# Kernel tuning notes

Hardware: AMD Instinct MI355X
Metric: run time of the kernel (lower is better)

The kernel has to match this reference:

```python
import jax, jax.numpy as jnp
import numpy as np

B, S, D, H = 8, 512, 1024, 8
DPH = D // H            # 128, dim per head
MAX_REL = 32
NGRAM = 2               # 2-gram RNN on heads 4..7
NG_START, NG_COUNT = 4, 4
SCALE = float(DPH) ** 0.5


def setup_inputs() -> dict:
    key = jax.random.key(0)
    ks = jax.random.split(key, 12)
    w = lambda k, shp: jax.random.normal(k, shp, jnp.float32) * 0.02
    return {
        "x": jax.random.normal(ks[0], (B, S, D), jnp.float32),
        "mask": jax.random.randint(ks[1], (B, 1, S), 0, 2).astype(bool),
        "Wq": w(ks[2], (D, D)), "bq": jnp.zeros((D,), jnp.float32),
        "Wk": w(ks[3], (D, D)), "bk": jnp.zeros((D,), jnp.float32),
        "Wv": w(ks[4], (D, D)), "bv": jnp.zeros((D,), jnp.float32),
        "Wo": w(ks[5], (D, D)), "bo": jnp.zeros((D,), jnp.float32),
        "rel_emb": w(ks[6], (2 * MAX_REL + 1, DPH)),
        "Wih_f": w(ks[7], (DPH, DPH)), "Whh_f": w(ks[8], (DPH, DPH)),
        "bih_f": jnp.zeros((DPH,), jnp.float32), "bhh_f": jnp.zeros((DPH,), jnp.float32),
        "Wih_b": w(ks[9], (DPH, DPH)), "Whh_b": w(ks[10], (DPH, DPH)),
        "bih_b": jnp.zeros((DPH,), jnp.float32), "bhh_b": jnp.zeros((DPH,), jnp.float32),
    }


def reference(x, mask, Wq, bq, Wk, bk, Wv, bv, Wo, bo, rel_emb,
              Wih_f, Whh_f, bih_f, bhh_f, Wih_b, Whh_b, bih_b, bhh_b):
    shape_h = lambda t: t.reshape(B, S, H, DPH).transpose(0, 2, 1, 3)  # [B,H,S,d]
    q = shape_h(x @ Wq.T + bq)
    k = shape_h(x @ Wk.T + bk)
    v = shape_h(x @ Wv.T + bv)

    # --- ngram path: zero masked positions in q/k/v (all heads) ---
    m = mask[:, :, :, None]  # [B,1,S,1] broadcast over heads and d
    q = jnp.where(m, 0.0, q)
    k = jnp.where(m, 0.0, k)
    v = jnp.where(m, 0.0, v)

    # per-head 2-gram bidirectional RNN on heads NG_START..NG_START+NG_COUNT-1
    qh = q[:, NG_START:NG_START + NG_COUNT].reshape(-1, S, DPH)
    kh = k[:, NG_START:NG_START + NG_COUNT].reshape(-1, S, DPH)
    vh = v[:, NG_START:NG_START + NG_COUNT].reshape(-1, S, DPH)
    feats = jnp.concatenate([qh, kh, vh], axis=0)          # [3*B*NG_COUNT, S, d]
    shifted = jnp.pad(feats, ((0, 0), (1, 0), (0, 0)))[:, :-1]  # shift-by-1 (prev token)
    seq = jnp.stack([shifted, feats], axis=0).reshape(NGRAM, -1, DPH)  # [T, N*S, d]
    h0 = jnp.zeros((seq.shape[1], DPH), jnp.float32)
    fstep = lambda h, xt: (jnp.tanh(xt @ Wih_f.T + bih_f + h @ Whh_f.T + bhh_f), None)
    bstep = lambda h, xt: (jnp.tanh(xt @ Wih_b.T + bih_b + h @ Whh_b.T + bhh_b), None)
    hf, _ = jax.lax.scan(fstep, h0, seq)            # fwd final hidden
    hb, _ = jax.lax.scan(bstep, h0, seq[::-1])      # bwd final hidden
    yy = (hf + hb).reshape(3, B, NG_COUNT, S, DPH)  # sum of direction finals
    q = q.at[:, NG_START:NG_START + NG_COUNT].set(yy[0])
    k = k.at[:, NG_START:NG_START + NG_COUNT].set(yy[1])
    v = v.at[:, NG_START:NG_START + NG_COUNT].set(yy[2])

    # --- relative-position attention ---
    qs = q / SCALE
    r = jnp.arange(S)
    rel_idx = jnp.clip(r[None, :] - r[:, None], -MAX_REL, MAX_REL) + MAX_REL  # [S,S]
    rel_k = rel_emb[rel_idx]  # [S,S,d]; same table used for keys and values
    scores = jnp.einsum('bhqd,bhkd->bhqk', qs, k) + jnp.einsum('bhqd,qkd->bhqk', qs, rel_k)
    scores = jnp.where(mask[:, None], -1e18, scores)  # [B,1,1,S] broadcast
    attn = jax.nn.softmax(scores, axis=-1)
    ctx = jnp.einsum('bhqk,bhkd->bhqd', attn, v) + jnp.einsum('bhqk,qkd->bhqd', attn, rel_k)
    out = ctx.transpose(0, 2, 1, 3).reshape(B, S, D) @ Wo.T + bo
    return out, attn
```

## Files before the change

### kernel.cpp

```cpp
#include <hip/hip_runtime.h>


typedef __bf16 bf16x8 __attribute__((ext_vector_type(8)));
typedef float f32x4 __attribute__((ext_vector_type(4)));

#define MFMA16(a, b, c) __builtin_amdgcn_mfma_f32_16x16x32_bf16(a, b, c, 0, 0, 0)

__device__ __forceinline__ unsigned short f2bf(float f) {
  unsigned u = __float_as_uint(f);
  u += 0x7FFFu + ((u >> 16) & 1u);
  return (unsigned short)(u >> 16);
}
__device__ __forceinline__ uint2 pack4(float4 f) {
  uint2 r;
  r.x = (unsigned)f2bf(f.x) | ((unsigned)f2bf(f.y) << 16);
  r.y = (unsigned)f2bf(f.z) | ((unsigned)f2bf(f.w) << 16);
  return r;
}
__device__ __forceinline__ void gld16(const unsigned short* g, unsigned short* l) {
  __builtin_amdgcn_global_load_lds(
      (const __attribute__((address_space(1))) unsigned int*)g,
      (__attribute__((address_space(3))) unsigned int*)l, 16, 0, 0);
}

__global__ __launch_bounds__(256) void prep_bf16(
    const float* __restrict__ x,
    const float* __restrict__ Wq, const float* __restrict__ Wk,
    const float* __restrict__ Wv,
    const float* __restrict__ Wihf, const float* __restrict__ Whhf,
    const float* __restrict__ Wihb, const float* __restrict__ Whhb,
    unsigned short* __restrict__ xb, unsigned short* __restrict__ Wqkvb,
    unsigned short* __restrict__ Wrnnb) {
  int i = blockIdx.x * 256 + threadIdx.x;
  const float* src;
  unsigned short* dst;
  int off;
  if (i < 1048576) {
    src = x; dst = xb; off = i;
  } else if (i < 1310720) {
    src = Wq; dst = Wqkvb; off = i - 1048576;
  } else if (i < 1572864) {
    src = Wk; dst = Wqkvb + 1048576; off = i - 1310720;
  } else if (i < 1835008) {
    src = Wv; dst = Wqkvb + 2097152; off = i - 1572864;
  } else if (i < 1839104) {
    src = Wihf; dst = Wrnnb; off = i - 1835008;
  } else if (i < 1843200) {
    src = Whhf; dst = Wrnnb + 16384; off = i - 1839104;
  } else if (i < 1847296) {
    src = Wihb; dst = Wrnnb + 32768; off = i - 1843200;
  } else {
    src = Whhb; dst = Wrnnb + 49152; off = i - 1847296;
  }
  float4 f = *((const float4*)src + off);
  *(uint2*)(dst + (size_t)off * 4) = pack4(f);
}

__global__ __launch_bounds__(256) void qkv_proj(
    const unsigned short* __restrict__ xb, const unsigned short* __restrict__ Wqkvb,
    const float* __restrict__ bq, const float* __restrict__ bk,
    const float* __restrict__ bv, const int* __restrict__ mask,
    unsigned short* __restrict__ qb, unsigned short* __restrict__ kb,
    unsigned short* __restrict__ vb, unsigned short* __restrict__ vT) {
  __shared__ __align__(16) unsigned short As[128 * 64];
  __shared__ __align__(16) unsigned short Bs[128 * 64];
  const int bm = blockIdx.x & 31;
  const int bn = blockIdx.x >> 5;
  const int t = bn >> 3;
  const int nloc0 = (bn & 7) * 128;
  const unsigned short* W = Wqkvb + (size_t)t * 1048576;
  const float* bias = (t == 0) ? bq : (t == 1) ? bk : bv;
  const int tid = threadIdx.x;
  const int lane = tid & 63, w = tid >> 6;
  const int wm = (w >> 1) * 64, wn = (w & 1) * 64;
  const int lanelo = lane & 15, quad = lane >> 4;
  const int row0 = bm * 128;
  const int rloc = lane >> 3, pch = lane & 7;
  const int lch = (pch - rloc) & 7;

  f32x4 acc[4][4];
  const f32x4 zf = {0.f, 0.f, 0.f, 0.f};
#pragma unroll
  for (int i = 0; i < 4; ++i)
#pragma unroll
    for (int j = 0; j < 4; ++j) acc[i][j] = zf;

  for (int kt = 0; kt < 16; ++kt) {
#pragma unroll
    for (int q = 0; q < 4; ++q) {
      int seg = w * 4 + q;
      int grow = seg * 8 + rloc;
      gld16(xb + (size_t)(row0 + grow) * 1024 + kt * 64 + lch * 8, &As[seg * 512]);
      gld16(W + (size_t)(nloc0 + grow) * 1024 + kt * 64 + lch * 8, &Bs[seg * 512]);
    }
    __syncthreads();
#pragma unroll
    for (int ks = 0; ks < 2; ++ks) {
      const int pA = (ks * 4 + quad + lanelo) & 7;
      bf16x8 a[4], bb[4];
#pragma unroll
      for (int i = 0; i < 4; ++i)
        a[i] = *(const bf16x8*)(&As[(wm + i * 16 + lanelo) * 64 + pA * 8]);
#pragma unroll
      for (int j = 0; j < 4; ++j)
        bb[j] = *(const bf16x8*)(&Bs[(wn + j * 16 + lanelo) * 64 + pA * 8]);
#pragma unroll
      for (int i = 0; i < 4; ++i)
#pragma unroll
        for (int j = 0; j < 4; ++j) acc[i][j] = MFMA16(a[i], bb[j], acc[i][j]);
    }
    __syncthreads();
  }
#pragma unroll
  for (int i = 0; i < 4; ++i) {
#pragma unroll
    for (int j = 0; j < 4; ++j) {
      int jj = nloc0 + wn + j * 16 + lanelo;
      int hh = jj >> 7, dc = jj & 127;
      float bvv = bias[jj];
      int m0 = row0 + wm + i * 16 + quad * 4;
      int b0 = m0 >> 9, sS = m0 & 511;
      unsigned short ov[4];
#pragma unroll
      for (int r = 0; r < 4; ++r) {
        int s = sS + r;
        float val = acc[i][j][r] + bvv;
        if (mask[b0 * 512 + s]) val = 0.f;
        unsigned short o = f2bf(val);
        ov[r] = o;
        size_t off = ((size_t)(b0 * 8 + hh) * 512 + s) * 128 + dc;
        if (t == 0) qb[off] = o;
        else if (t == 1) kb[off] = o;
        else vb[off] = o;
      }
      if (t == 2) {
        uint2 pk;
        pk.x = (unsigned)ov[0] | ((unsigned)ov[1] << 16);
        pk.y = (unsigned)ov[2] | ((unsigned)ov[3] << 16);
        *(uint2*)(&vT[((size_t)(b0 * 8 + hh) * 128 + dc) * 512 + sS]) = pk;
      }
    }
  }
}

__global__ __launch_bounds__(256) void prep_rel(
    const float* __restrict__ rel, unsigned short* __restrict__ relb,
    unsigned short* __restrict__ relT) {
  int i = blockIdx.x * 256 + threadIdx.x;
  if (i < 65 * 128) relb[i] = f2bf(rel[i]);
  if (i < 128 * 96) {
    int d = i / 96, r = i - d * 96;
    relT[i] = (r < 65) ? f2bf(rel[r * 128 + d]) : (unsigned short)0;
  }
}

__global__ __launch_bounds__(256) void rnn_fused(
    const unsigned short* __restrict__ qb, const unsigned short* __restrict__ kb,
    const unsigned short* __restrict__ vb,
    const unsigned short* __restrict__ Wrnnb,
    const float* __restrict__ bihf, const float* __restrict__ bhhf,
    const float* __restrict__ bihb, const float* __restrict__ bhhb,
    unsigned short* __restrict__ rnn_out) {
  __shared__ __align__(16) unsigned short X[65 * 136];
  __shared__ __align__(16) unsigned short Wi[128 * 136];
  __shared__ __align__(16) unsigned short Wh[128 * 136];
  __shared__ __align__(16) unsigned short H1[64 * 136];
  __shared__ float cbf[128], cbb[128];

  const unsigned short* Wihfb = Wrnnb;
  const unsigned short* Whhfb = Wrnnb + 16384;
  const unsigned short* Wihbb = Wrnnb + 32768;
  const unsigned short* Whhbb = Wrnnb + 49152;

  const int gid = blockIdx.x;
  const int tile = gid & 7;
  const int g = gid >> 3;
  const int t = g >> 5;
  const int rem = g & 31;
  const int b = rem >> 2, h = (rem & 3) + 4;
  const int s0 = tile * 64;
  const unsigned short* src = (t == 0) ? qb : (t == 1) ? kb : vb;
  const size_t rowbase = (size_t)(b * 8 + h) * 512;
  const int tid = threadIdx.x;

  for (int c = tid; c < 65 * 16; c += 256) {
    int r = c >> 4, cc = c & 15;
    uint4 v4;
    if (r == 0 && s0 == 0) v4 = make_uint4(0, 0, 0, 0);
    else v4 = *(const uint4*)(src + (rowbase + (s0 - 1 + r)) * 128 + cc * 8);
    *(uint4*)(&X[r * 136 + cc * 8]) = v4;
  }
#pragma unroll
  for (int p = 0; p < 8; ++p) {
    int c = p * 256 + tid;
    int r = c >> 4, cc = c & 15;
    *(uint4*)(&Wi[r * 136 + cc * 8]) = *(const uint4*)(Wihfb + c * 8);
    *(uint4*)(&Wh[r * 136 + cc * 8]) = *(const uint4*)(Whhfb + c * 8);
  }
  if (tid < 128) {
    cbf[tid] = bihf[tid] + bhhf[tid];
    cbb[tid] = bihb[tid] + bhhb[tid];
  }
  __syncthreads();

  const int lane = tid & 63, w = tid >> 6;
  const int lanelo = lane & 15, quad = lane >> 4;
  const int marow = w * 16 + lanelo;
  const f32x4 zf = {0.f, 0.f, 0.f, 0.f};

  f32x4 g1[8];
#pragma unroll
  for (int j = 0; j < 8; ++j) g1[j] = zf;
#pragma unroll
  for (int ks = 0; ks < 4; ++ks) {
    bf16x8 a = *(const bf16x8*)(&X[marow * 136 + ks * 32 + quad * 8]);
#pragma unroll
    for (int j = 0; j < 8; ++j) {
      bf16x8 bb = *(const bf16x8*)(&Wi[(j * 16 + lanelo) * 136 + ks * 32 + quad * 8]);
      g1[j] = MFMA16(a, bb, g1[j]);
    }
  }
#pragma unroll
  for (int j = 0; j < 8; ++j) {
    int col = j * 16 + lanelo;
    float cb = cbf[col];
#pragma unroll
    for (int i = 0; i < 4; ++i) {
      int row = w * 16 + quad * 4 + i;
      H1[row * 136 + col] = f2bf(tanhf(g1[j][i] + cb));
    }
  }
  __syncthreads();
  f32x4 a2[8];
#pragma unroll
  for (int j = 0; j < 8; ++j) a2[j] = zf;
#pragma unroll
  for (int ks = 0; ks < 4; ++ks) {
    bf16x8 a = *(const bf16x8*)(&X[(marow + 1) * 136 + ks * 32 + quad * 8]);
#pragma unroll
    for (int j = 0; j < 8; ++j) {
      bf16x8 bb = *(const bf16x8*)(&Wi[(j * 16 + lanelo) * 136 + ks * 32 + quad * 8]);
      a2[j] = MFMA16(a, bb, a2[j]);
    }
  }
#pragma unroll
  for (int ks = 0; ks < 4; ++ks) {
    bf16x8 a = *(const bf16x8*)(&H1[marow * 136 + ks * 32 + quad * 8]);
#pragma unroll
    for (int j = 0; j < 8; ++j) {
      bf16x8 bb = *(const bf16x8*)(&Wh[(j * 16 + lanelo) * 136 + ks * 32 + quad * 8]);
      a2[j] = MFMA16(a, bb, a2[j]);
    }
  }
  float outF[8][4];
#pragma unroll
  for (int j = 0; j < 8; ++j) {
    int col = j * 16 + lanelo;
    float cb = cbf[col];
#pragma unroll
    for (int i = 0; i < 4; ++i) outF[j][i] = tanhf(a2[j][i] + cb);
  }
  __syncthreads();
#pragma unroll
  for (int p = 0; p < 8; ++p) {
    int c = p * 256 + tid;
    int r = c >> 4, cc = c & 15;
    *(uint4*)(&Wi[r * 136 + cc * 8]) = *(const uint4*)(Wihbb + c * 8);
    *(uint4*)(&Wh[r * 136 + cc * 8]) = *(const uint4*)(Whhbb + c * 8);
  }
  __syncthreads();
#pragma unroll
  for (int j = 0; j < 8; ++j) g1[j] = zf;
#pragma unroll
  for (int ks = 0; ks < 4; ++ks) {
    bf16x8 a = *(const bf16x8*)(&X[(marow + 1) * 136 + ks * 32 + quad * 8]);
#pragma unroll
    for (int j = 0; j < 8; ++j) {
      bf16x8 bb = *(const bf16x8*)(&Wi[(j * 16 + lanelo) * 136 + ks * 32 + quad * 8]);
      g1[j] = MFMA16(a, bb, g1[j]);
    }
  }
#pragma unroll
  for (int j = 0; j < 8; ++j) {
    int col = j * 16 + lanelo;
    float cb = cbb[col];
#pragma unroll
    for (int i = 0; i < 4; ++i) {
      int row = w * 16 + quad * 4 + i;
      H1[row * 136 + col] = f2bf(tanhf(g1[j][i] + cb));
    }
  }
  __syncthreads();
#pragma unroll
  for (int j = 0; j < 8; ++j) a2[j] = zf;
#pragma unroll
  for (int ks = 0; ks < 4; ++ks) {
    bf16x8 a = *(const bf16x8*)(&X[marow * 136 + ks * 32 + quad * 8]);
#pragma unroll
    for (int j = 0; j < 8; ++j) {
      bf16x8 bb = *(const bf16x8*)(&Wi[(j * 16 + lanelo) * 136 + ks * 32 + quad * 8]);
      a2[j] = MFMA16(a, bb, a2[j]);
    }
  }
#pragma unroll
  for (int ks = 0; ks < 4; ++ks) {
    bf16x8 a = *(const bf16x8*)(&H1[marow * 136 + ks * 32 + quad * 8]);
#pragma unroll
    for (int j = 0; j < 8; ++j) {
      bf16x8 bb = *(const bf16x8*)(&Wh[(j * 16 + lanelo) * 136 + ks * 32 + quad * 8]);
      a2[j] = MFMA16(a, bb, a2[j]);
    }
  }
#pragma unroll
  for (int j = 0; j < 8; ++j) {
    int col = j * 16 + lanelo;
    float cb = cbb[col];
#pragma unroll
    for (int i = 0; i < 4; ++i) {
      int row = w * 16 + quad * 4 + i;
      float val = outF[j][i] + tanhf(a2[j][i] + cb);
      rnn_out[((size_t)g * 512 + s0 + row) * 128 + col] = f2bf(val);
    }
  }
}

__global__ __launch_bounds__(256) void rnn_copyback(
    const unsigned short* __restrict__ rnn_out,
    unsigned short* __restrict__ qb, unsigned short* __restrict__ kb,
    unsigned short* __restrict__ vT) {
  int idx = blockIdx.x * 256 + threadIdx.x;
  int g = idx >> 16;
  int r2 = idx & 65535;
  int s = r2 >> 7, col = r2 & 127;
  int t = g >> 5, rem = g & 31, b = rem >> 2, h = (rem & 3) + 4;
  unsigned short val = rnn_out[idx];
  size_t off = ((size_t)(b * 8 + h) * 512 + s) * 128 + col;
  if (t == 0) qb[off] = val;
  else if (t == 1) kb[off] = val;
  else vT[((size_t)(b * 8 + h) * 128 + col) * 512 + s] = val;
}

__global__ __launch_bounds__(256) void scores_av_fused(
    const unsigned short* __restrict__ qbuf, const unsigned short* __restrict__ kbuf,
    const unsigned short* __restrict__ relb, const unsigned short* __restrict__ vT,
    const unsigned short* __restrict__ relT, const float* __restrict__ relf,
    const int* __restrict__ mask, float* __restrict__ attn_out,
    unsigned short* __restrict__ ctx) {
  __shared__ __align__(16) char smem[81920];
  unsigned short* As = (unsigned short*)smem;
  unsigned short* Bs = (unsigned short*)(smem + 17408);
  float* Ps = (float*)(smem + 50176);
  float* cmaskS = (float*)(smem + 71680);
  unsigned short* abufT = (unsigned short*)(smem + 73728);
  unsigned short* attnb = (unsigned short*)smem;
  unsigned short* Bs2 = (unsigned short*)(smem + 65536);
  float* redb = (float*)(smem + 65536);

  const int idx = blockIdx.x;
  const int qt = idx >> 6, bh = idx & 63, b = bh >> 3;
  const int q0 = qt * 64;
  const size_t qrow0 = (size_t)bh * 512 + q0;
  const int tid = threadIdx.x;
  const int lane = tid & 63, w = tid >> 6;
  const int lanelo = lane & 15, quad = lane >> 4;
  const int rloc4 = lane >> 2, pch4 = lane & 3;
  const int lch4 = (pch4 - rloc4) & 3;
  const int pB = (quad + lanelo) & 3;
  const f32x4 zf = {0.f, 0.f, 0.f, 0.f};

  for (int c = tid; c < 1024; c += 256) {
    int r = c >> 4, cc = c & 15;
    *(uint4*)(&As[r * 136 + cc * 8]) = *(const uint4*)(qbuf + (qrow0 + r) * 128 + cc * 8);
  }
  for (int i = tid; i < 512; i += 256) cmaskS[i] = mask[b * 512 + i] ? -1e9f : 0.f;
  for (int i = tid; i < 512; i += 256) *(uint4*)(&abufT[i * 8]) = make_uint4(0, 0, 0, 0);
  __syncthreads();

  f32x4 pacc[5];
#pragma unroll
  for (int j = 0; j < 5; ++j) pacc[j] = zf;
  for (int ks = 0; ks < 4; ++ks) {
    for (int c = tid; c < 320; c += 256) {
      int r = c >> 2, cc = c & 3;
      uint4 v4 = (r < 65) ? *(const uint4*)(relb + r * 128 + ks * 32 + cc * 8)
                          : make_uint4(0, 0, 0, 0);
      *(uint4*)(&Bs[r * 32 + ((cc + r) & 3) * 8]) = v4;
    }
    __syncthreads();
    bf16x8 qf_ = *(const bf16x8*)(&As[(w * 16 + lanelo) * 136 + ks * 32 + quad * 8]);
#pragma unroll
    for (int j = 0; j < 5; ++j) {
      bf16x8 rf_ = *(const bf16x8*)(&Bs[(j * 16 + lanelo) * 32 + pB * 8]);
      pacc[j] = MFMA16(rf_, qf_, pacc[j]);
    }
    __syncthreads();
  }
#pragma unroll
  for (int j = 0; j < 5; ++j)
    *(f32x4*)(&Ps[(w * 16 + lanelo) * 84 + j * 16 + quad * 4]) = pacc[j];

  f32x4 acc[8][4];
#pragma unroll
  for (int kf = 0; kf < 8; ++kf)
#pragma unroll
    for (int nf = 0; nf < 4; ++nf) acc[kf][nf] = zf;
  for (int ks = 0; ks < 4; ++ks) {
#pragma unroll
    for (int qq = 0; qq < 8; ++qq) {
      int seg = w * 8 + qq;
      int grow = seg * 16 + rloc4;
      gld16(kbuf + ((size_t)bh * 512 + grow) * 128 + ks * 32 + lch4 * 8,
            &Bs[seg * 512]);
    }
    __syncthreads();
    bf16x8 qfr[4];
#pragma unroll
    for (int nf = 0; nf < 4; ++nf)
      qfr[nf] = *(const bf16x8*)(&As[(nf * 16 + lanelo) * 136 + ks * 32 + quad * 8]);
#pragma unroll
    for (int kf = 0; kf < 8; ++kf) {
      bf16x8 kfr = *(const bf16x8*)(&Bs[((w * 8 + kf) * 16 + lanelo) * 32 + pB * 8]);
#pragma unroll
      for (int nf = 0; nf < 4; ++nf) acc[kf][nf] = MFMA16(kfr, qfr[nf], acc[kf][nf]);
    }
    __syncthreads();
  }

  const float rscale = 0.08838834764831845f;
  float pmax[4] = {-3e38f, -3e38f, -3e38f, -3e38f};
#pragma unroll
  for (int qf = 0; qf < 4; ++qf) {
    const int q = qf * 16 + lanelo;
    const int qg = q0 + q;
    const float* PsR = &Ps[q * 84];
#pragma unroll
    for (int kf = 0; kf < 8; ++kf) {
      const int kbase = w * 128 + kf * 16 + quad * 4;
#pragma unroll
      for (int i = 0; i < 4; ++i) {
        int k = kbase + i;
        int d = k - qg;
        int r = min(max(d, -32), 32) + 32;
        float val = (acc[kf][qf][i] + PsR[r]) * rscale + cmaskS[k];
        acc[kf][qf][i] = val;
        pmax[qf] = fmaxf(pmax[qf], val);
      }
    }
  }
  float* red_max = redb;
  float* red_sum = redb + 256;
  float* red_s0 = redb + 512;
  float* red_s64 = redb + 768;
#pragma unroll
  for (int qf = 0; qf < 4; ++qf) {
    pmax[qf] = fmaxf(pmax[qf], __shfl_xor(pmax[qf], 16, 64));
    pmax[qf] = fmaxf(pmax[qf], __shfl_xor(pmax[qf], 32, 64));
  }
  if (quad == 0) {
#pragma unroll
    for (int qf = 0; qf < 4; ++qf) red_max[w * 64 + qf * 16 + lanelo] = pmax[qf];
  }
  __syncthreads();
  float mf_[4], psum[4];
#pragma unroll
  for (int qf = 0; qf < 4; ++qf) {
    int q = qf * 16 + lanelo;
    mf_[qf] = fmaxf(fmaxf(red_max[q], red_max[64 + q]),
                    fmaxf(red_max[128 + q], red_max[192 + q]));
    psum[qf] = 0.f;
  }
#pragma unroll
  for (int qf = 0; qf < 4; ++qf)
#pragma unroll
    for (int kf = 0; kf < 8; ++kf)
#pragma unroll
      for (int i = 0; i < 4; ++i) {
        float e = __expf(acc[kf][qf][i] - mf_[qf]);
        acc[kf][qf][i] = e;
        psum[qf] += e;
      }
#pragma unroll
  for (int qf = 0; qf < 4; ++qf) {
    psum[qf] += __shfl_xor(psum[qf], 16, 64);
    psum[qf] += __shfl_xor(psum[qf], 32, 64);
  }
  if (quad == 0) {
#pragma unroll
    for (int qf = 0; qf < 4; ++qf) red_sum[w * 64 + qf * 16 + lanelo] = psum[qf];
  }
  __syncthreads();
  float rs[4];
#pragma unroll
  for (int qf = 0; qf < 4; ++qf) {
    int q = qf * 16 + lanelo;
    float s = red_sum[q] + red_sum[64 + q] + red_sum[128 + q] + red_sum[192 + q];
    rs[qf] = (s > 0.f) ? 1.f / s : 0.f;
  }

  float s0p[4] = {0.f, 0.f, 0.f, 0.f}, s64p[4] = {0.f, 0.f, 0.f, 0.f};
#pragma unroll
  for (int qf = 0; qf < 4; ++qf) {
    const int q = qf * 16 + lanelo;
    const int qg = q0 + q;
#pragma unroll
    for (int kf = 0; kf < 8; ++kf) {
      const int kbase = w * 128 + kf * 16 + quad * 4;
      float4 at;
      float* ap = (float*)&at;
#pragma unroll
      for (int i = 0; i < 4; ++i) {
        float v = acc[kf][qf][i] * rs[qf];
        ap[i] = v;
        int d = kbase + i - qg;
        if (d <= -32) s0p[qf] += v;
        else if (d >= 32) s64p[qf] += v;
        else {
          int col = d + 32;
          abufT[q * 64 + (((col >> 3) + q) & 7) * 8 + (col & 7)] = f2bf(v);
        }
      }
      *(float4*)(&attn_out[((size_t)bh * 512 + qg) * 512 + kbase]) = at;
      uint2 pk = pack4(at);
      int cc = kbase >> 3;
      *(uint2*)(&attnb[q * 512 + ((cc + q) & 63) * 8 + (quad & 1) * 4]) = pk;
    }
  }
#pragma unroll
  for (int qf = 0; qf < 4; ++qf) {
    s0p[qf] += __shfl_xor(s0p[qf], 16, 64);
    s0p[qf] += __shfl_xor(s0p[qf], 32, 64);
    s64p[qf] += __shfl_xor(s64p[qf], 16, 64);
    s64p[qf] += __shfl_xor(s64p[qf], 32, 64);
  }
  if (quad == 0) {
#pragma unroll
    for (int qf = 0; qf < 4; ++qf) {
      red_s0[w * 64 + qf * 16 + lanelo] = s0p[qf];
      red_s64[w * 64 + qf * 16 + lanelo] = s64p[qf];
    }
  }
  __syncthreads();
  float s0f[4], s64f[4];
#pragma unroll
  for (int qf = 0; qf < 4; ++qf) {
    int q = qf * 16 + lanelo;
    s0f[qf] = red_s0[q] + red_s0[64 + q] + red_s0[128 + q] + red_s0[192 + q];
    s64f[qf] = red_s64[q] + red_s64[64 + q] + red_s64[128 + q] + red_s64[192 + q];
  }
  __syncthreads();

  f32x4 cacc[2][4];
#pragma unroll
  for (int mf = 0; mf < 2; ++mf)
#pragma unroll
    for (int nf = 0; nf < 4; ++nf) cacc[mf][nf] = zf;
  for (int kt = 0; kt < 18; ++kt) {
#pragma unroll
    for (int qq = 0; qq < 2; ++qq) {
      int seg = w * 2 + qq;
      int grow = seg * 16 + rloc4;
      if (kt < 16)
        gld16(vT + ((size_t)bh * 128 + grow) * 512 + kt * 32 + lch4 * 8, &Bs2[seg * 512]);
      else
        gld16(relT + grow * 96 + (kt - 16) * 32 + lch4 * 8, &Bs2[seg * 512]);
    }
    __syncthreads();
    bf16x8 afr[2], bfr[4];
#pragma unroll
    for (int mf = 0; mf < 2; ++mf)
      afr[mf] = *(const bf16x8*)(&Bs2[((w * 2 + mf) * 16 + lanelo) * 32 + pB * 8]);
    if (kt < 16) {
#pragma unroll
      for (int nf = 0; nf < 4; ++nf) {
        int q = nf * 16 + lanelo;
        bfr[nf] = *(const bf16x8*)(&attnb[q * 512 + ((kt * 4 + quad + q) & 63) * 8]);
      }
    } else {
#pragma unroll
      for (int nf = 0; nf < 4; ++nf) {
        int q = nf * 16 + lanelo;
        bfr[nf] = *(const bf16x8*)(&abufT[q * 64 + (((kt - 16) * 4 + quad + q) & 7) * 8]);
      }
    }
#pragma unroll
    for (int mf = 0; mf < 2; ++mf)
#pragma unroll
      for (int nf = 0; nf < 4; ++nf) cacc[mf][nf] = MFMA16(afr[mf], bfr[nf], cacc[mf][nf]);
    __syncthreads();
  }

  float r0v[2][4], r64v[2][4];
#pragma unroll
  for (int mf = 0; mf < 2; ++mf)
#pragma unroll
    for (int i = 0; i < 4; ++i) {
      int d = w * 32 + mf * 16 + quad * 4 + i;
      r0v[mf][i] = relf[d];
      r64v[mf][i] = relf[64 * 128 + d];
    }
  const int b_ = bh >> 3, h_ = bh & 7;
#pragma unroll
  for (int nf = 0; nf < 4; ++nf) {
    int qg = q0 + nf * 16 + lanelo;
#pragma unroll
    for (int mf = 0; mf < 2; ++mf) {
      unsigned short ov[4];
#pragma unroll
      for (int i = 0; i < 4; ++i) {
        float val = cacc[mf][nf][i] + s0f[nf] * r0v[mf][i] + s64f[nf] * r64v[mf][i];
        ov[i] = f2bf(val);
      }
      uint2 pk;
      pk.x = (unsigned)ov[0] | ((unsigned)ov[1] << 16);
      pk.y = (unsigned)ov[2] | ((unsigned)ov[3] << 16);
      *(uint2*)(&ctx[((size_t)(b_ * 512 + qg)) * 1024 + h_ * 128 + w * 32 + mf * 16 + quad * 4]) = pk;
    }
  }
}

__global__ __launch_bounds__(256) void out_proj(
    const unsigned short* __restrict__ ctx, const float* __restrict__ Wo,
    const float* __restrict__ bo, float* __restrict__ outp) {
  __shared__ __align__(16) unsigned short As[128 * 64];
  __shared__ __align__(16) unsigned short Bs[128 * 64];
  const int bm = blockIdx.x & 31, bn = blockIdx.x >> 5;
  const int tid = threadIdx.x, lane = tid & 63, w = tid >> 6;
  const int wm = (w >> 1) * 64, wn = (w & 1) * 64;
  const int lanelo = lane & 15, quad = lane >> 4;
  const int row0 = bm * 128, col0 = bn * 128;
  const int rloc = lane >> 3, pch = lane & 7;
  const int lch = (pch - rloc) & 7;
  f32x4 acc[4][4];
  const f32x4 zf = {0.f, 0.f, 0.f, 0.f};
#pragma unroll
  for (int i = 0; i < 4; ++i)
#pragma unroll
    for (int j = 0; j < 4; ++j) acc[i][j] = zf;

  for (int kt = 0; kt < 16; ++kt) {
#pragma unroll
    for (int q = 0; q < 4; ++q) {
      int seg = w * 4 + q;
      int grow = seg * 8 + rloc;
      gld16(ctx + (size_t)(row0 + grow) * 1024 + kt * 64 + lch * 8, &As[seg * 512]);
    }
    for (int c = tid; c < 1024; c += 256) {
      int r = c >> 3, cc2 = c & 7;
      const float* src = Wo + (size_t)(col0 + r) * 1024 + kt * 64 + cc2 * 8;
      int pc = (cc2 + r) & 7;
      *(uint2*)(&Bs[r * 64 + pc * 8]) = pack4(*(const float4*)src);
      *(uint2*)(&Bs[r * 64 + pc * 8 + 4]) = pack4(*(const float4*)(src + 4));
    }
    __syncthreads();
#pragma unroll
    for (int ks = 0; ks < 2; ++ks) {
      const int pA = (ks * 4 + quad + lanelo) & 7;
      bf16x8 a[4], bb[4];
#pragma unroll
      for (int i = 0; i < 4; ++i)
        a[i] = *(const bf16x8*)(&As[(wm + i * 16 + lanelo) * 64 + pA * 8]);
#pragma unroll
      for (int j = 0; j < 4; ++j)
        bb[j] = *(const bf16x8*)(&Bs[(wn + j * 16 + lanelo) * 64 + pA * 8]);
#pragma unroll
      for (int i = 0; i < 4; ++i)
#pragma unroll
        for (int j = 0; j < 4; ++j) acc[i][j] = MFMA16(a[i], bb[j], acc[i][j]);
    }
    __syncthreads();
  }
#pragma unroll
  for (int i = 0; i < 4; ++i) {
#pragma unroll
    for (int j = 0; j < 4; ++j) {
      int n = col0 + wn + j * 16 + lanelo;
      float bbv = bo[n];
#pragma unroll
      for (int r = 0; r < 4; ++r) {
        int m = row0 + wm + i * 16 + quad * 4 + r;
        outp[(size_t)m * 1024 + n] = acc[i][j][r] + bbv;
      }
    }
  }
}

extern "C" void kernel_launch(void* const* d_in, const int* in_sizes, int n_in,
                              void* d_out, int out_size, void* d_ws, size_t ws_size,
                              hipStream_t stream) {
  const float* x    = (const float*)d_in[0];
  const int*   mask = (const int*)d_in[1];
  const float* Wq   = (const float*)d_in[2];
  const float* bq   = (const float*)d_in[3];
  const float* Wk   = (const float*)d_in[4];
  const float* bk   = (const float*)d_in[5];
  const float* Wv   = (const float*)d_in[6];
  const float* bv   = (const float*)d_in[7];
  const float* Wo   = (const float*)d_in[8];
  const float* bo   = (const float*)d_in[9];
  const float* rel  = (const float*)d_in[10];
  const float* Wihf = (const float*)d_in[11];
  const float* Whhf = (const float*)d_in[12];
  const float* bihf = (const float*)d_in[13];
  const float* bhhf = (const float*)d_in[14];
  const float* Wihb = (const float*)d_in[15];
  const float* Whhb = (const float*)d_in[16];
  const float* bihb = (const float*)d_in[17];
  const float* bhhb = (const float*)d_in[18];

  char* ws = (char*)d_ws;
  unsigned short* qb   = (unsigned short*)(ws + 0);
  unsigned short* kb   = (unsigned short*)(ws + 8388608);
  unsigned short* vT   = (unsigned short*)(ws + 16777216);
  unsigned short* ctx  = (unsigned short*)(ws + 25165824);
  unsigned short* relb = (unsigned short*)(ws + 33554432);
  unsigned short* relT = (unsigned short*)(ws + 33571072);

  float* outp  = (float*)d_out;
  float* attnF = outp + 4194304;
  unsigned short* abase  = (unsigned short*)attnF;
  unsigned short* xb     = abase;
  unsigned short* vb     = abase + 4194304;
  unsigned short* rnnout = abase + 8388608;
  unsigned short* Wqkvb  = abase + 14680064;
  unsigned short* Wrnnb  = abase + 17825792;

  prep_bf16<<<dim3(7232), dim3(256), 0, stream>>>(
      x, Wq, Wk, Wv, Wihf, Whhf, Wihb, Whhb, xb, Wqkvb, Wrnnb);
  prep_rel<<<dim3(48), dim3(256), 0, stream>>>(rel, relb, relT);
  qkv_proj<<<dim3(768), dim3(256), 0, stream>>>(xb, Wqkvb, bq, bk, bv, mask,
                                                qb, kb, vb, vT);
  rnn_fused<<<dim3(768), dim3(256), 0, stream>>>(qb, kb, vb, Wrnnb,
                                                 bihf, bhhf, bihb, bhhb, rnnout);
  rnn_copyback<<<dim3(24576), dim3(256), 0, stream>>>(rnnout, qb, kb, vT);
  scores_av_fused<<<dim3(512), dim3(256), 0, stream>>>(qb, kb, relb, vT, relT,
                                                       rel, mask, attnF, ctx);
  out_proj<<<dim3(256), dim3(256), 0, stream>>>(ctx, Wo, bo, outp);
}
```

Baseline: 373.1 us.

## Load K, V and rel fragments directly from global into registers, drop LDS staging

```diff
diff --git a/kernel.cpp b/kernel.cpp
--- a/kernel.cpp
+++ b/kernel.cpp
@@ -346,15 +346,13 @@
     const unsigned short* __restrict__ relT, const float* __restrict__ relf,
     const int* __restrict__ mask, float* __restrict__ attn_out,
     unsigned short* __restrict__ ctx) {
-  __shared__ __align__(16) char smem[81920];
+  __shared__ __align__(16) char smem[77824];
   unsigned short* As = (unsigned short*)smem;
-  unsigned short* Bs = (unsigned short*)(smem + 17408);
-  float* Ps = (float*)(smem + 50176);
-  float* cmaskS = (float*)(smem + 71680);
-  unsigned short* abufT = (unsigned short*)(smem + 73728);
+  float* Ps = (float*)(smem + 17408);
+  float* cmaskS = (float*)(smem + 38912);
   unsigned short* attnb = (unsigned short*)smem;
-  unsigned short* Bs2 = (unsigned short*)(smem + 65536);
-  float* redb = (float*)(smem + 65536);
+  unsigned short* abufT = (unsigned short*)(smem + 65536);
+  float* redb = (float*)(smem + 73728);
 
   const int idx = blockIdx.x;
   const int qt = idx >> 6, bh = idx & 63, b = bh >> 3;
@@ -363,9 +361,6 @@
   const int tid = threadIdx.x;
   const int lane = tid & 63, w = tid >> 6;
   const int lanelo = lane & 15, quad = lane >> 4;
-  const int rloc4 = lane >> 2, pch4 = lane & 3;
-  const int lch4 = (pch4 - rloc4) & 3;
-  const int pB = (quad + lanelo) & 3;
   const f32x4 zf = {0.f, 0.f, 0.f, 0.f};
 
   for (int c = tid; c < 1024; c += 256) {
@@ -379,51 +374,44 @@
   f32x4 pacc[5];
 #pragma unroll
   for (int j = 0; j < 5; ++j) pacc[j] = zf;
+#pragma unroll
   for (int ks = 0; ks < 4; ++ks) {
-    for (int c = tid; c < 320; c += 256) {
-      int r = c >> 2, cc = c & 3;
-      uint4 v4 = (r < 65) ? *(const uint4*)(relb + r * 128 + ks * 32 + cc * 8)
-                          : make_uint4(0, 0, 0, 0);
-      *(uint4*)(&Bs[r * 32 + ((cc + r) & 3) * 8]) = v4;
-    }
-    __syncthreads();
     bf16x8 qf_ = *(const bf16x8*)(&As[(w * 16 + lanelo) * 136 + ks * 32 + quad * 8]);
 #pragma unroll
     for (int j = 0; j < 5; ++j) {
-      bf16x8 rf_ = *(const bf16x8*)(&Bs[(j * 16 + lanelo) * 32 + pB * 8]);
+      int r = j * 16 + lanelo;
+      uint4 tmp = make_uint4(0, 0, 0, 0);
+      if (r < 65) tmp = *(const uint4*)(relb + r * 128 + ks * 32 + quad * 8);
+      bf16x8 rf_ = *(bf16x8*)&tmp;
       pacc[j] = MFMA16(rf_, qf_, pacc[j]);
     }
-    __syncthreads();
   }
 #pragma unroll
   for (int j = 0; j < 5; ++j)
     *(f32x4*)(&Ps[(w * 16 + lanelo) * 84 + j * 16 + quad * 4]) = pacc[j];
+  __syncthreads();
 
   f32x4 acc[8][4];
 #pragma unroll
   for (int kf = 0; kf < 8; ++kf)
 #pragma unroll
     for (int nf = 0; nf < 4; ++nf) acc[kf][nf] = zf;
+  const unsigned short* kbp = kbuf + (size_t)bh * 65536;
+#pragma unroll
   for (int ks = 0; ks < 4; ++ks) {
-#pragma unroll
-    for (int qq = 0; qq < 8; ++qq) {
-      int seg = w * 8 + qq;
-      int grow = seg * 16 + rloc4;
-      gld16(kbuf + ((size_t)bh * 512 + grow) * 128 + ks * 32 + lch4 * 8,
-            &Bs[seg * 512]);
-    }
-    __syncthreads();
     bf16x8 qfr[4];
 #pragma unroll
     for (int nf = 0; nf < 4; ++nf)
       qfr[nf] = *(const bf16x8*)(&As[(nf * 16 + lanelo) * 136 + ks * 32 + quad * 8]);
-#pragma unroll
-    for (int kf = 0; kf < 8; ++kf) {
-      bf16x8 kfr = *(const bf16x8*)(&Bs[((w * 8 + kf) * 16 + lanelo) * 32 + pB * 8]);
-#pragma unroll
-      for (int nf = 0; nf < 4; ++nf) acc[kf][nf] = MFMA16(kfr, qfr[nf], acc[kf][nf]);
-    }
-    __syncthreads();
+    bf16x8 kfr[8];
+#pragma unroll
+    for (int kf = 0; kf < 8; ++kf)
+      kfr[kf] = *(const bf16x8*)(kbp + (size_t)((w * 8 + kf) * 16 + lanelo) * 128 +
+                                 ks * 32 + quad * 8);
+#pragma unroll
+    for (int kf = 0; kf < 8; ++kf)
+#pragma unroll
+      for (int nf = 0; nf < 4; ++nf) acc[kf][nf] = MFMA16(kfr[kf], qfr[nf], acc[kf][nf]);
   }
 
   const float rscale = 0.08838834764831845f;
@@ -433,17 +421,36 @@
     const int q = qf * 16 + lanelo;
     const int qg = q0 + q;
     const float* PsR = &Ps[q * 84];
+    const float p0 = PsR[0], p64 = PsR[64];
+    const int qgmin = q0 + qf * 16;
 #pragma unroll
     for (int kf = 0; kf < 8; ++kf) {
-      const int kbase = w * 128 + kf * 16 + quad * 4;
-#pragma unroll
-      for (int i = 0; i < 4; ++i) {
-        int k = kbase + i;
-        int d = k - qg;
-        int r = min(max(d, -32), 32) + 32;
-        float val = (acc[kf][qf][i] + PsR[r]) * rscale + cmaskS[k];
-        acc[kf][qf][i] = val;
-        pmax[qf] = fmaxf(pmax[qf], val);
+      const int kmin = w * 128 + kf * 16;
+      const int kbase = kmin + quad * 4;
+      if (kmin + 15 - qgmin <= -32) {
+#pragma unroll
+        for (int i = 0; i < 4; ++i) {
+          float val = (acc[kf][qf][i] + p0) * rscale + cmaskS[kbase + i];
+          acc[kf][qf][i] = val;
+          pmax[qf] = fmaxf(pmax[qf], val);
+        }
+      } else if (kmin - (qgmin + 15) >= 32) {
+#pragma unroll
+        for (int i = 0; i < 4; ++i) {
+          float val = (acc[kf][qf][i] + p64) * rscale + cmaskS[kbase + i];
+          acc[kf][qf][i] = val;
+          pmax[qf] = fmaxf(pmax[qf], val);
+        }
+      } else {
+#pragma unroll
+        for (int i = 0; i < 4; ++i) {
+          int k = kbase + i;
+          int d = k - qg;
+          int r = min(max(d, -32), 32) + 32;
+          float val = (acc[kf][qf][i] + PsR[r]) * rscale + cmaskS[k];
+          acc[kf][qf][i] = val;
+          pmax[qf] = fmaxf(pmax[qf], val);
+        }
       }
     }
   }
@@ -502,21 +509,31 @@
   for (int qf = 0; qf < 4; ++qf) {
     const int q = qf * 16 + lanelo;
     const int qg = q0 + q;
+    const int qgmin = q0 + qf * 16;
 #pragma unroll
     for (int kf = 0; kf < 8; ++kf) {
-      const int kbase = w * 128 + kf * 16 + quad * 4;
+      const int kmin = w * 128 + kf * 16;
+      const int kbase = kmin + quad * 4;
       float4 at;
       float* ap = (float*)&at;
 #pragma unroll
-      for (int i = 0; i < 4; ++i) {
-        float v = acc[kf][qf][i] * rs[qf];
-        ap[i] = v;
-        int d = kbase + i - qg;
-        if (d <= -32) s0p[qf] += v;
-        else if (d >= 32) s64p[qf] += v;
-        else {
-          int col = d + 32;
-          abufT[q * 64 + (((col >> 3) + q) & 7) * 8 + (col & 7)] = f2bf(v);
+      for (int i = 0; i < 4; ++i) ap[i] = acc[kf][qf][i] * rs[qf];
+      if (kmin + 15 - qgmin <= -32) {
+#pragma unroll
+        for (int i = 0; i < 4; ++i) s0p[qf] += ap[i];
+      } else if (kmin - (qgmin + 15) >= 32) {
+#pragma unroll
+        for (int i = 0; i < 4; ++i) s64p[qf] += ap[i];
+      } else {
+#pragma unroll
+        for (int i = 0; i < 4; ++i) {
+          int d = kbase + i - qg;
+          if (d <= -32) s0p[qf] += ap[i];
+          else if (d >= 32) s64p[qf] += ap[i];
+          else {
+            int col = d + 32;
+            abufT[q * 64 + (((col >> 3) + q) & 7) * 8 + (col & 7)] = f2bf(ap[i]);
+          }
         }
       }
       *(float4*)(&attn_out[((size_t)bh * 512 + qg) * 512 + kbase]) = at;
@@ -547,46 +564,46 @@
     s0f[qf] = red_s0[q] + red_s0[64 + q] + red_s0[128 + q] + red_s0[192 + q];
     s64f[qf] = red_s64[q] + red_s64[64 + q] + red_s64[128 + q] + red_s64[192 + q];
   }
-  __syncthreads();
 
   f32x4 cacc[2][4];
 #pragma unroll
   for (int mf = 0; mf < 2; ++mf)
 #pragma unroll
     for (int nf = 0; nf < 4; ++nf) cacc[mf][nf] = zf;
-  for (int kt = 0; kt < 18; ++kt) {
-#pragma unroll
-    for (int qq = 0; qq < 2; ++qq) {
-      int seg = w * 2 + qq;
-      int grow = seg * 16 + rloc4;
-      if (kt < 16)
-        gld16(vT + ((size_t)bh * 128 + grow) * 512 + kt * 32 + lch4 * 8, &Bs2[seg * 512]);
-      else
-        gld16(relT + grow * 96 + (kt - 16) * 32 + lch4 * 8, &Bs2[seg * 512]);
-    }
-    __syncthreads();
+  const unsigned short* vbp = vT + (size_t)bh * 65536;
+#pragma unroll
+  for (int kt = 0; kt < 16; ++kt) {
     bf16x8 afr[2], bfr[4];
 #pragma unroll
     for (int mf = 0; mf < 2; ++mf)
-      afr[mf] = *(const bf16x8*)(&Bs2[((w * 2 + mf) * 16 + lanelo) * 32 + pB * 8]);
-    if (kt < 16) {
-#pragma unroll
-      for (int nf = 0; nf < 4; ++nf) {
-        int q = nf * 16 + lanelo;
-        bfr[nf] = *(const bf16x8*)(&attnb[q * 512 + ((kt * 4 + quad + q) & 63) * 8]);
-      }
-    } else {
-#pragma unroll
-      for (int nf = 0; nf < 4; ++nf) {
-        int q = nf * 16 + lanelo;
-        bfr[nf] = *(const bf16x8*)(&abufT[q * 64 + (((kt - 16) * 4 + quad + q) & 7) * 8]);
-      }
+      afr[mf] = *(const bf16x8*)(vbp + (size_t)((w * 2 + mf) * 16 + lanelo) * 512 +
+                                 kt * 32 + quad * 8);
+#pragma unroll
+    for (int nf = 0; nf < 4; ++nf) {
+      int q = nf * 16 + lanelo;
+      bfr[nf] = *(const bf16x8*)(&attnb[q * 512 + ((kt * 4 + quad + q) & 63) * 8]);
     }
 #pragma unroll
     for (int mf = 0; mf < 2; ++mf)
 #pragma unroll
       for (int nf = 0; nf < 4; ++nf) cacc[mf][nf] = MFMA16(afr[mf], bfr[nf], cacc[mf][nf]);
-    __syncthreads();
+  }
+#pragma unroll
+  for (int kt = 16; kt < 18; ++kt) {
+    bf16x8 afr[2], bfr[4];
+#pragma unroll
+    for (int mf = 0; mf < 2; ++mf)
+      afr[mf] = *(const bf16x8*)(relT + ((w * 2 + mf) * 16 + lanelo) * 96 +
+                                 (kt - 16) * 32 + quad * 8);
+#pragma unroll
+    for (int nf = 0; nf < 4; ++nf) {
+      int q = nf * 16 + lanelo;
+      bfr[nf] = *(const bf16x8*)(&abufT[q * 64 + (((kt - 16) * 4 + quad + q) & 7) * 8]);
+    }
+#pragma unroll
+    for (int mf = 0; mf < 2; ++mf)
+#pragma unroll
+      for (int nf = 0; nf < 4; ++nf) cacc[mf][nf] = MFMA16(afr[mf], bfr[nf], cacc[mf][nf]);
   }
 
   float r0v[2][4], r64v[2][4];
```

Result: faster. 364.1 us (-2.4%).
